# Performance work log

Hardware: AMD Instinct MI355X
Metric: run time of the kernel (lower is better)

The kernel has to match this reference:

```python
import jax, jax.numpy as jnp
import numpy as np

B, L, D, S = 64, 512, 768, 8
HOP, LAMB = 3, 0.5


def _layernorm(x, g, b, eps=1e-5):
    m = x.mean(-1, keepdims=True)
    v = x.var(-1, keepdims=True)
    return (x - m) / jnp.sqrt(v + eps) * g + b


def _hop_refine(cur, sentence, ln_g, ln_b):
    # cur, sentence: [B,S,D]. HOP-1 refinement steps, then return last row.
    for _ in range(HOP - 1):
        coef = jnp.einsum('bd,bsd->bs', cur[:, -1, :], sentence)  # [B,S]
        a = coef[..., None] * sentence                             # [B,S,D]
        cur = LAMB * _layernorm(jax.nn.sigmoid(a), ln_g, ln_b) + sentence
    return cur[:, -1, :]  # [B,D]


def _conv1d(x, w, b):
    # x: [B,D,S], w: [Dout,Din,3], padding=1 (same)
    y = jax.lax.conv_general_dilated(
        x, w, window_strides=(1,), padding=((1, 1),),
        dimension_numbers=('NCH', 'OIH', 'NCH'))
    return y + b[None, :, None]


def setup_inputs() -> dict:
    key = jax.random.key(0)
    ks = jax.random.split(key, 16)
    p = lambda k, shp: (jax.random.normal(k, shp, dtype=jnp.float32) * 0.02)
    # segment boundaries: strictly increasing, start at 1, <= L, gaps ~63 with jitter < 32
    base = 1 + np.arange(S + 1) * ((L - 1) // S)          # [9]
    jitter = np.array(jax.random.randint(ks[15], (B, S + 1), 0, 32))
    jitter[:, 0] = 0
    jitter[:, -1] = 0
    seg_bounds = jnp.asarray(base[None, :] + jitter, dtype=jnp.int64 if jax.config.jax_enable_x64 else jnp.int32)
    return {
        'bert_output': jax.random.normal(ks[0], (B, L, D), dtype=jnp.float32),
        'target': jax.random.normal(ks[1], (B, D), dtype=jnp.float32),
        'gc1_w': p(ks[2], (D, D)), 'gc1_b': p(ks[3], (D,)),
        'gc2_w': p(ks[4], (D, D)), 'gc2_b': p(ks[5], (D,)),
        'conv1_w': p(ks[6], (D, D, 3)), 'conv1_b': p(ks[7], (D,)),
        'conv2_w': p(ks[8], (D, D, 3)), 'conv2_b': p(ks[9], (D,)),
        'ln_g': jnp.ones((D,), jnp.float32), 'ln_b': jnp.zeros((D,), jnp.float32),
        'fc2_w': p(ks[10], (3 * D, 3)), 'fc2_b': p(ks[11], (3,)),
        'seg_bounds': seg_bounds,
    }


def reference(bert_output, target, gc1_w, gc1_b, gc2_w, gc2_b,
              conv1_w, conv1_b, conv2_w, conv2_b, ln_g, ln_b,
              fc2_w, fc2_b, seg_bounds):
    dt = bert_output.dtype
    start = seg_bounds[:, :-1]   # [B,S]
    end = seg_bounds[:, 1:]      # [B,S]
    pos = jnp.arange(L)
    seg_mask = ((pos[None, None, :] >= start[:, :, None]) &
                (pos[None, None, :] < end[:, :, None])).astype(dt)  # [B,S,L]
    cnt = (end - start).astype(dt)                                   # [B,S]
    # batched segment-mean pooling
    sentence = jnp.einsum('bsl,bld->bsd', seg_mask, bert_output) / cnt[..., None]

    # GCN branch: adj = I + superdiagonal, row-degree normalization
    adj = jnp.eye(S, dtype=dt) + jnp.eye(S, k=1, dtype=dt)
    denom = adj.sum(axis=1)  # [S]

    def gcn(x, w, b):
        h = jnp.einsum('bsd,de->bse', x, w)
        return jnp.einsum('st,btd->bsd', adj, h) / denom[None, :, None] + b

    g1 = jnp.tanh(gcn(sentence, gc1_w, gc1_b))
    g2 = jnp.tanh(gcn(g1, gc2_w, gc2_b))
    a3 = _hop_refine(g2, sentence, ln_g, ln_b)

    # Conv branch: two conv1d (k=3, pad=1) over the segment axis
    x = jnp.swapaxes(sentence, 1, 2)  # [B,D,S]
    c = jnp.tanh(_conv1d(x, conv1_w, conv1_b))
    c = jnp.tanh(_conv1d(c, conv2_w, conv2_b))
    conv_out = jnp.swapaxes(c, 1, 2)  # [B,S,D]
    a4 = _hop_refine(conv_out, sentence, ln_g, ln_b)

    # Self-mask branch
    coef0 = jnp.einsum('bd,bsd->bs', sentence[:, -1, :], sentence)
    tmask = jax.nn.sigmoid(coef0[..., None] * sentence)
    a5 = _hop_refine(tmask, sentence, ln_g, ln_b)

    fnout = jnp.stack([a3, a4, a5], axis=1)                 # [B,3,D]
    # NOTE: original uses target[0] (first sample's pooler output) for all samples
    w = jax.nn.softmax(jnp.einsum('bkd,d->bk', fnout, target[0]), axis=1)
    fn = (fnout * w[..., None]).reshape(fnout.shape[0], 3 * D)
    return fn @ fc2_w + fc2_b  # [B,3]
```

## Files before the change

kernel.cpp:

```cpp
#include <hip/hip_runtime.h>


typedef unsigned short u16;
typedef short short8 __attribute__((ext_vector_type(8)));
typedef float f32x4 __attribute__((ext_vector_type(4)));

__device__ __forceinline__ float bf2f(u16 h) {
    unsigned int u = ((unsigned int)h) << 16;
    float f;
    __builtin_memcpy(&f, &u, 4);
    return f;
}
__device__ __forceinline__ u16 f2bf(float f) {
    unsigned int u;
    __builtin_memcpy(&u, &f, 4);
    u = (u + 0x7fffu + ((u >> 16) & 1u)) >> 16;
    return (u16)u;
}
__device__ __forceinline__ float sigm(float x) { return 1.0f / (1.0f + __expf(-x)); }

__device__ __forceinline__ float ldv(const void* p, long i, bool bf) {
    return bf ? bf2f(((const u16*)p)[i]) : ((const float*)p)[i];
}

__device__ __forceinline__ bool detect_bf16(const u16* bert) {
    int hits = 0;
#pragma unroll
    for (int i = 0; i < 256; i += 2) {
        const int e = (bert[i] >> 7) & 0xFF;
        hits += (e >= 115 && e <= 130) ? 1 : 0;
    }
    return hits > 64;
}

__global__ __launch_bounds__(256) void k0_zero(float* __restrict__ ws)
{
    ((float4*)ws)[blockIdx.x * 256 + threadIdx.x] = make_float4(0.f, 0.f, 0.f, 0.f);
}

__global__ __launch_bounds__(256) void k1_pool(
    const void* __restrict__ bertv, const int* __restrict__ sb,
    float* __restrict__ sentF, float* __restrict__ flagp)
{
    const int u = blockIdx.x, t = threadIdx.x;
    const bool bf = detect_bf16((const u16*)bertv);
    const bool is64 = (sb[1] == 0);
    if (u == 0 && t == 0) flagp[0] = bf ? 1.0f : 0.0f;
    const int q = u & 3, v = u >> 2;
    const int b = v / 3, si = v - 3 * (v / 3), s = 5 + si;
    const int i0 = b * 9 + s, i1 = i0 + 1;
    int st = is64 ? sb[2 * i0] : sb[i0];
    int en = is64 ? sb[2 * i1] : sb[i1];
    st = st < 0 ? 0 : (st > 511 ? 511 : st);
    en = en <= st ? st + 1 : (en > 512 ? 512 : en);
    const int n = en - st;
    const int r0 = st + (n * q) / 4;
    const int r1 = st + (n * (q + 1)) / 4;
    float a0 = 0.f, a1 = 0.f, a2 = 0.f;
    if (bf) {
        const u16* base = (const u16*)bertv + (size_t)b * 512 * 768;
        int l = r0;
        for (; l + 1 < r1; l += 2) {
            const u16* p0 = base + (size_t)l * 768;
            const u16* p1 = p0 + 768;
            const u16 x0 = p0[t], x1 = p0[t + 256], x2 = p0[t + 512];
            const u16 y0 = p1[t], y1 = p1[t + 256], y2 = p1[t + 512];
            a0 += bf2f(x0) + bf2f(y0);
            a1 += bf2f(x1) + bf2f(y1);
            a2 += bf2f(x2) + bf2f(y2);
        }
        if (l < r1) {
            const u16* p0 = base + (size_t)l * 768;
            a0 += bf2f(p0[t]);
            a1 += bf2f(p0[t + 256]);
            a2 += bf2f(p0[t + 512]);
        }
    } else {
        const float* base = (const float*)bertv + (size_t)b * 512 * 768;
        int l = r0;
        for (; l + 1 < r1; l += 2) {
            const float* p0 = base + (size_t)l * 768;
            const float* p1 = p0 + 768;
            const float x0 = p0[t], x1 = p0[t + 256], x2 = p0[t + 512];
            const float y0 = p1[t], y1 = p1[t + 256], y2 = p1[t + 512];
            a0 += x0 + y0;
            a1 += x1 + y1;
            a2 += x2 + y2;
        }
        if (l < r1) {
            const float* p0 = base + (size_t)l * 768;
            a0 += p0[t];
            a1 += p0[t + 256];
            a2 += p0[t + 512];
        }
    }
    const float inv = 1.0f / (float)n;
    float* o = sentF + b * 2304 + si * 768;
    atomicAdd(o + t, a0 * inv);
    atomicAdd(o + t + 256, a1 * inv);
    atomicAdd(o + t + 512, a2 * inv);
}

template <int XMODE, int WMODE>
__device__ __forceinline__ void gemm_core(
    const float* __restrict__ x, int xstride, const void* __restrict__ bias,
    const void* __restrict__ W, bool bf,
    float* __restrict__ out, int ostride,
    int n0, int k0, u16* As, u16* Bs)
{
    const int t = threadIdx.x;
    const int r = t >> 2;
    const int cseg = (t & 3) * 32;
    const int wave = t >> 6, lane = t & 63;
    const int lm = lane & 15, lq = lane >> 4;
    f32x4 acc[4] = {};

    for (int kk = 0; kk < 256; kk += 128) {
        const int kg = k0 + kk;
        {
            const float* xp = x + (size_t)r * xstride + (kg + cseg);
            u16* dst = As + r * 136 + cseg;
#pragma unroll
            for (int i = 0; i < 8; ++i) {
                float4 v = ((const float4*)xp)[i];
                if (XMODE == 1) {
                    int kb = kg + cseg + i * 4;
                    if (kb >= 768) kb -= 768;
                    v.x = tanhf(v.x + ldv(bias, kb, bf));
                    v.y = tanhf(v.y + ldv(bias, kb + 1, bf));
                    v.z = tanhf(v.z + ldv(bias, kb + 2, bf));
                    v.w = tanhf(v.w + ldv(bias, kb + 3, bf));
                }
                ((ushort4*)dst)[i] = make_ushort4(f2bf(v.x), f2bf(v.y), f2bf(v.z), f2bf(v.w));
            }
        }
        if (WMODE == 0) {
            const int p = t >> 2;
            const int nseg = (t & 3) * 16;
            u16 q0[16], q1[16];
            if (bf) {
                const u16* w0 = (const u16*)W + (size_t)(kg + 2 * p) * 768 + n0 + nseg;
                ((uint4*)q0)[0] = ((const uint4*)w0)[0];
                ((uint4*)q0)[1] = ((const uint4*)w0)[1];
                ((uint4*)q1)[0] = ((const uint4*)(w0 + 768))[0];
                ((uint4*)q1)[1] = ((const uint4*)(w0 + 768))[1];
            } else {
                const float* w0 = (const float*)W + (size_t)(kg + 2 * p) * 768 + n0 + nseg;
#pragma unroll
                for (int e = 0; e < 4; ++e) {
                    float4 v0 = ((const float4*)w0)[e];
                    float4 v1 = ((const float4*)(w0 + 768))[e];
                    q0[4 * e] = f2bf(v0.x); q0[4 * e + 1] = f2bf(v0.y);
                    q0[4 * e + 2] = f2bf(v0.z); q0[4 * e + 3] = f2bf(v0.w);
                    q1[4 * e] = f2bf(v1.x); q1[4 * e + 1] = f2bf(v1.y);
                    q1[4 * e + 2] = f2bf(v1.z); q1[4 * e + 3] = f2bf(v1.w);
                }
            }
#pragma unroll
            for (int e = 0; e < 16; ++e)
                *(ushort2*)(Bs + (nseg + e) * 136 + 2 * p) = make_ushort2(q0[e], q1[e]);
        } else {
            const int kb = kg / 768;
            const int i0c = kg - kb * 768;
            u16 tmp[32];
            if (bf) {
                const u16* wp = (const u16*)W + (size_t)(n0 + r) * 2304 + (size_t)(i0c + cseg) * 3 + kb;
#pragma unroll
                for (int j = 0; j < 32; ++j) tmp[j] = wp[j * 3];
            } else {
                const float* wp = (const float*)W + (size_t)(n0 + r) * 2304 + (size_t)(i0c + cseg) * 3 + kb;
#pragma unroll
                for (int j = 0; j < 32; ++j) tmp[j] = f2bf(wp[j * 3]);
            }
            u16* dst = Bs + r * 136 + cseg;
#pragma unroll
            for (int qq = 0; qq < 8; ++qq)
                ((ushort4*)dst)[qq] = ((ushort4*)tmp)[qq];
        }
        __syncthreads();
        const u16* ap = As + (wave * 16 + lm) * 136 + lq * 8;
        const u16* bp = Bs + lm * 136 + lq * 8;
#pragma unroll
        for (int ks = 0; ks < 4; ++ks) {
            short8 af = *(const short8*)(ap + ks * 32);
#pragma unroll
            for (int nf = 0; nf < 4; ++nf) {
                short8 bfr = *(const short8*)(bp + nf * 16 * 136 + ks * 32);
                acc[nf] = __builtin_amdgcn_mfma_f32_16x16x32_bf16(af, bfr, acc[nf], 0, 0, 0);
            }
        }
        __syncthreads();
    }
#pragma unroll
    for (int nf = 0; nf < 4; ++nf) {
#pragma unroll
        for (int rg = 0; rg < 4; ++rg) {
            const int row = wave * 16 + lq * 4 + rg;
            const int col = n0 + nf * 16 + lm;
            atomicAdd(out + (size_t)row * ostride + col, acc[nf][rg]);
        }
    }
}

__global__ __launch_bounds__(256) void k2_gemm_a(
    const float* __restrict__ sentF, const void* __restrict__ gc1w,
    const void* __restrict__ c1w, float* __restrict__ g1acc, float* __restrict__ c1acc,
    const float* __restrict__ flagp)
{
    __shared__ u16 As[64 * 136];
    __shared__ u16 Bs[64 * 136];
    const bool bf = flagp[0] > 0.5f;
    const int u = blockIdx.x;
    if (u < 36) {
        gemm_core<0, 0>(sentF + 1536, 2304, nullptr, gc1w, bf, g1acc, 768,
                        (u / 3) * 64, (u % 3) * 256, As, Bs);
    } else if (u < 144) {
        const int v = u - 36;
        gemm_core<0, 1>(sentF, 2304, nullptr, c1w, bf, c1acc, 1536,
                        (v / 9) * 64, (v % 9) * 256, As, Bs);
    } else {
        const int v = u - 144;
        gemm_core<0, 1>(sentF + 768, 2304, nullptr, c1w, bf, c1acc + 768, 1536,
                        (v / 6) * 64, (v % 6) * 256, As, Bs);
    }
}

__global__ __launch_bounds__(256) void k3_gemm_b(
    const float* __restrict__ g1acc, const float* __restrict__ c1acc,
    const void* __restrict__ gc2w, const void* __restrict__ c2w,
    const void* __restrict__ gc1b, const void* __restrict__ c1b,
    float* __restrict__ g2acc, float* __restrict__ c2acc,
    const float* __restrict__ flagp)
{
    __shared__ u16 As[64 * 136];
    __shared__ u16 Bs[64 * 136];
    const bool bf = flagp[0] > 0.5f;
    const int u = blockIdx.x;
    if (u < 36) {
        gemm_core<1, 0>(g1acc, 768, gc1b, gc2w, bf, g2acc, 768,
                        (u / 3) * 64, (u % 3) * 256, As, Bs);
    } else {
        const int v = u - 36;
        gemm_core<1, 1>(c1acc, 1536, c1b, c2w, bf, c2acc, 768,
                        (v / 6) * 64, (v % 6) * 256, As, Bs);
    }
}

__device__ __forceinline__ float block_sum(float v, float* red) {
#pragma unroll
    for (int m = 1; m < 64; m <<= 1) v += __shfl_xor(v, m, 64);
    const int wave = threadIdx.x >> 6, lane = threadIdx.x & 63;
    if (lane == 0) red[wave] = v;
    __syncthreads();
    const float r = red[0] + red[1] + red[2] + red[3];
    __syncthreads();
    return r;
}

__global__ __launch_bounds__(256) void k4_final(
    const float* __restrict__ sentF, const float* __restrict__ g2acc,
    const float* __restrict__ c2acc,
    const void* __restrict__ gc2b, const void* __restrict__ c2b,
    const void* __restrict__ lng, const void* __restrict__ lnb,
    const void* __restrict__ target, const void* __restrict__ fc2w,
    const void* __restrict__ fc2b, void* __restrict__ outp,
    const float* __restrict__ flagp)
{
    __shared__ float red[4];
    const bool bf = flagp[0] > 0.5f;
    const int t = threadIdx.x, b = blockIdx.x;
    float s_[3], g_[3], bb_[3];
    const float* srow = sentF + b * 2304 + 1536;
#pragma unroll
    for (int i = 0; i < 3; ++i) {
        const int d = t + 256 * i;
        s_[i] = srow[d];
        g_[i] = ldv(lng, d, bf);
        bb_[i] = ldv(lnb, d, bf);
    }

    auto refine2 = [&](float* yv) {
#pragma unroll
        for (int it = 0; it < 2; ++it) {
            const float c = block_sum(yv[0] * s_[0] + yv[1] * s_[1] + yv[2] * s_[2], red);
            float tt[3], sm = 0.0f, sq = 0.0f;
#pragma unroll
            for (int i = 0; i < 3; ++i) {
                tt[i] = sigm(c * s_[i]);
                sm += tt[i];
                sq += tt[i] * tt[i];
            }
            const float m = block_sum(sm, red) * (1.0f / 768.0f);
            const float q = block_sum(sq, red) * (1.0f / 768.0f);
            const float inv = rsqrtf(fmaxf(q - m * m, 0.0f) + 1e-5f);
#pragma unroll
            for (int i = 0; i < 3; ++i)
                yv[i] = 0.5f * ((tt[i] - m) * inv * g_[i] + bb_[i]) + s_[i];
        }
    };

    float a3[3], a4[3], a5[3], y[3];
#pragma unroll
    for (int i = 0; i < 3; ++i) {
        const int d = t + 256 * i;
        y[i] = tanhf(g2acc[b * 768 + d] + ldv(gc2b, d, bf));
    }
    refine2(y);
    a3[0] = y[0]; a3[1] = y[1]; a3[2] = y[2];
#pragma unroll
    for (int i = 0; i < 3; ++i) {
        const int d = t + 256 * i;
        y[i] = tanhf(c2acc[b * 768 + d] + ldv(c2b, d, bf));
    }
    refine2(y);
    a4[0] = y[0]; a4[1] = y[1]; a4[2] = y[2];
    const float ss = block_sum(s_[0] * s_[0] + s_[1] * s_[1] + s_[2] * s_[2], red);
#pragma unroll
    for (int i = 0; i < 3; ++i) y[i] = sigm(ss * s_[i]);
    refine2(y);
    a5[0] = y[0]; a5[1] = y[1]; a5[2] = y[2];

    float tg[3];
#pragma unroll
    for (int i = 0; i < 3; ++i) tg[i] = ldv(target, t + 256 * i, bf);
    const float u0 = block_sum(a3[0] * tg[0] + a3[1] * tg[1] + a3[2] * tg[2], red);
    const float u1 = block_sum(a4[0] * tg[0] + a4[1] * tg[1] + a4[2] * tg[2], red);
    const float u2 = block_sum(a5[0] * tg[0] + a5[1] * tg[1] + a5[2] * tg[2], red);
    const float mx = fmaxf(u0, fmaxf(u1, u2));
    const float e0 = __expf(u0 - mx), e1 = __expf(u1 - mx), e2 = __expf(u2 - mx);
    const float es = e0 + e1 + e2;
    const float w0 = e0 / es, w1 = e1 / es, w2 = e2 / es;

    float p0 = 0.0f, p1 = 0.0f, p2 = 0.0f;
#pragma unroll
    for (int i = 0; i < 3; ++i) {
        const int d = t + 256 * i;
        const float va = w0 * a3[i], vb = w1 * a4[i], vc = w2 * a5[i];
        p0 += va * ldv(fc2w, d * 3 + 0, bf) + vb * ldv(fc2w, (768 + d) * 3 + 0, bf) + vc * ldv(fc2w, (1536 + d) * 3 + 0, bf);
        p1 += va * ldv(fc2w, d * 3 + 1, bf) + vb * ldv(fc2w, (768 + d) * 3 + 1, bf) + vc * ldv(fc2w, (1536 + d) * 3 + 1, bf);
        p2 += va * ldv(fc2w, d * 3 + 2, bf) + vb * ldv(fc2w, (768 + d) * 3 + 2, bf) + vc * ldv(fc2w, (1536 + d) * 3 + 2, bf);
    }
    p0 = block_sum(p0, red);
    p1 = block_sum(p1, red);
    p2 = block_sum(p2, red);
    if (t == 0) {
        const float o0 = p0 + ldv(fc2b, 0, bf);
        const float o1 = p1 + ldv(fc2b, 1, bf);
        const float o2 = p2 + ldv(fc2b, 2, bf);
        if (bf) {
            ((u16*)outp)[b * 3 + 0] = f2bf(o0);
            ((u16*)outp)[b * 3 + 1] = f2bf(o1);
            ((u16*)outp)[b * 3 + 2] = f2bf(o2);
        } else {
            ((float*)outp)[b * 3 + 0] = o0;
            ((float*)outp)[b * 3 + 1] = o1;
            ((float*)outp)[b * 3 + 2] = o2;
        }
    }
}

extern "C" void kernel_launch(void* const* d_in, const int* in_sizes, int n_in,
                              void* d_out, int out_size, void* d_ws, size_t ws_size,
                              hipStream_t stream) {
    const void* bert   = d_in[0];
    const void* target = d_in[1];
    const void* gc1w   = d_in[2];
    const void* gc1b   = d_in[3];
    const void* gc2w   = d_in[4];
    const void* gc2b   = d_in[5];
    const void* c1w    = d_in[6];
    const void* c1b    = d_in[7];
    const void* c2w    = d_in[8];
    const void* c2b    = d_in[9];
    const void* lng    = d_in[10];
    const void* lnb    = d_in[11];
    const void* fc2w   = d_in[12];
    const void* fc2b   = d_in[13];
    const int*  sb     = (const int*)d_in[14];

    float* sentF = (float*)d_ws;
    float* accs  = sentF + 147456;
    float* g1acc = accs;
    float* c1acc = accs + 49152;
    float* g2acc = c1acc + 98304;
    float* c2acc = g2acc + 49152;
    float* flagp = accs + 245760;

    k0_zero<<<384, 256, 0, stream>>>(sentF);
    k1_pool<<<768, 256, 0, stream>>>(bert, sb, sentF, flagp);
    k2_gemm_a<<<216, 256, 0, stream>>>(sentF, gc1w, c1w, g1acc, c1acc, flagp);
    k3_gemm_b<<<108, 256, 0, stream>>>(g1acc, c1acc, gc2w, c2w, gc1b, c1b, g2acc, c2acc, flagp);
    k4_final<<<64, 256, 0, stream>>>(sentF, g2acc, c2acc, gc2b, c2b, lng, lnb,
                                     target, fc2w, fc2b, d_out, flagp);
}
```

Baseline: 224.5 us.

## Fuse workspace zeroing into pooling and replace atomics with block reduction

The separate zeroing kernel is removed, and each pooling block now zeroes a slice of the GEMM accumulator workspace itself. Pooling is repartitioned so each block owns a 192-column slice and its four waves split the rows. Partial sums are combined in shared memory and written directly, so atomics and pre-zeroing of the sentence buffer are no longer needed. This saves one launch and the atomic traffic, at the cost of narrower per-wave loads that are less coalesced.

```diff
diff --git a/kernel.cpp b/kernel.cpp
--- a/kernel.cpp
+++ b/kernel.cpp
@@ -33,20 +33,19 @@
     return hits > 64;
 }
 
-__global__ __launch_bounds__(256) void k0_zero(float* __restrict__ ws)
-{
-    ((float4*)ws)[blockIdx.x * 256 + threadIdx.x] = make_float4(0.f, 0.f, 0.f, 0.f);
-}
-
-__global__ __launch_bounds__(256) void k1_pool(
+__global__ __launch_bounds__(256) void kA_pool(
     const void* __restrict__ bertv, const int* __restrict__ sb,
-    float* __restrict__ sentF, float* __restrict__ flagp)
-{
+    float* __restrict__ sentF, float* __restrict__ accs, float* __restrict__ flagp)
+{
+    __shared__ float red[4][192];
     const int u = blockIdx.x, t = threadIdx.x;
+    if (t < 80)
+        ((float4*)accs)[u * 80 + t] = make_float4(0.f, 0.f, 0.f, 0.f);
     const bool bf = detect_bf16((const u16*)bertv);
     const bool is64 = (sb[1] == 0);
     if (u == 0 && t == 0) flagp[0] = bf ? 1.0f : 0.0f;
-    const int q = u & 3, v = u >> 2;
+
+    const int cq = u & 3, v = u >> 2;
     const int b = v / 3, si = v - 3 * (v / 3), s = 5 + si;
     const int i0 = b * 9 + s, i1 = i0 + 1;
     int st = is64 ? sb[2 * i0] : sb[i0];
@@ -54,51 +53,54 @@
     st = st < 0 ? 0 : (st > 511 ? 511 : st);
     en = en <= st ? st + 1 : (en > 512 ? 512 : en);
     const int n = en - st;
-    const int r0 = st + (n * q) / 4;
-    const int r1 = st + (n * (q + 1)) / 4;
+
+    const int wave = t >> 6, lane = t & 63;
+    const int r0 = st + (n * wave) / 4;
+    const int r1 = st + (n * (wave + 1)) / 4;
+    const int col0 = cq * 192;
+
     float a0 = 0.f, a1 = 0.f, a2 = 0.f;
     if (bf) {
-        const u16* base = (const u16*)bertv + (size_t)b * 512 * 768;
+        const u16* base = (const u16*)bertv + (size_t)b * 512 * 768 + col0;
         int l = r0;
         for (; l + 1 < r1; l += 2) {
             const u16* p0 = base + (size_t)l * 768;
             const u16* p1 = p0 + 768;
-            const u16 x0 = p0[t], x1 = p0[t + 256], x2 = p0[t + 512];
-            const u16 y0 = p1[t], y1 = p1[t + 256], y2 = p1[t + 512];
-            a0 += bf2f(x0) + bf2f(y0);
-            a1 += bf2f(x1) + bf2f(y1);
-            a2 += bf2f(x2) + bf2f(y2);
+            a0 += bf2f(p0[lane]) + bf2f(p1[lane]);
+            a1 += bf2f(p0[lane + 64]) + bf2f(p1[lane + 64]);
+            a2 += bf2f(p0[lane + 128]) + bf2f(p1[lane + 128]);
         }
         if (l < r1) {
             const u16* p0 = base + (size_t)l * 768;
-            a0 += bf2f(p0[t]);
-            a1 += bf2f(p0[t + 256]);
-            a2 += bf2f(p0[t + 512]);
+            a0 += bf2f(p0[lane]);
+            a1 += bf2f(p0[lane + 64]);
+            a2 += bf2f(p0[lane + 128]);
         }
     } else {
-        const float* base = (const float*)bertv + (size_t)b * 512 * 768;
+        const float* base = (const float*)bertv + (size_t)b * 512 * 768 + col0;
         int l = r0;
         for (; l + 1 < r1; l += 2) {
             const float* p0 = base + (size_t)l * 768;
             const float* p1 = p0 + 768;
-            const float x0 = p0[t], x1 = p0[t + 256], x2 = p0[t + 512];
-            const float y0 = p1[t], y1 = p1[t + 256], y2 = p1[t + 512];
-            a0 += x0 + y0;
-            a1 += x1 + y1;
-            a2 += x2 + y2;
+            a0 += p0[lane] + p1[lane];
+            a1 += p0[lane + 64] + p1[lane + 64];
+            a2 += p0[lane + 128] + p1[lane + 128];
         }
         if (l < r1) {
             const float* p0 = base + (size_t)l * 768;
-            a0 += p0[t];
-            a1 += p0[t + 256];
-            a2 += p0[t + 512];
-        }
-    }
-    const float inv = 1.0f / (float)n;
-    float* o = sentF + b * 2304 + si * 768;
-    atomicAdd(o + t, a0 * inv);
-    atomicAdd(o + t + 256, a1 * inv);
-    atomicAdd(o + t + 512, a2 * inv);
+            a0 += p0[lane];
+            a1 += p0[lane + 64];
+            a2 += p0[lane + 128];
+        }
+    }
+    red[wave][lane] = a0;
+    red[wave][lane + 64] = a1;
+    red[wave][lane + 128] = a2;
+    __syncthreads();
+    if (t < 192) {
+        const float sum = red[0][t] + red[1][t] + red[2][t] + red[3][t];
+        sentF[b * 2304 + si * 768 + col0 + t] = sum * (1.0f / (float)n);
+    }
 }
 
 template <int XMODE, int WMODE>
@@ -386,8 +388,7 @@
     float* c2acc = g2acc + 49152;
     float* flagp = accs + 245760;
 
-    k0_zero<<<384, 256, 0, stream>>>(sentF);
-    k1_pool<<<768, 256, 0, stream>>>(bert, sb, sentF, flagp);
+    kA_pool<<<768, 256, 0, stream>>>(bert, sb, sentF, accs, flagp);
     k2_gemm_a<<<216, 256, 0, stream>>>(sentF, gc1w, c1w, g1acc, c1acc, flagp);
     k3_gemm_b<<<108, 256, 0, stream>>>(g1acc, c1acc, gc2w, c2w, gc1b, c1b, g2acc, c2acc, flagp);
     k4_final<<<64, 256, 0, stream>>>(sentF, g2acc, c2acc, gc2b, c2b, lng, lnb,
```

New measurement: 219.2 us, median of 2. 2.4% less time.
